# Kernel tuning notes

Measured on AMD Instinct MI355X. Metric: run time of the kernel, lower is better.

## Reference

```python
import jax, jax.numpy as jnp
import numpy as np
from jax import lax

V, E, H, T, B = 32000, 512, 512, 64, 64

def _xavier(key, shape):
    fan_out, fan_in = shape
    std = np.sqrt(2.0 / (fan_in + fan_out))
    return jax.random.normal(key, shape, dtype=jnp.float32) * std

def setup_inputs() -> dict:
    key = jax.random.key(0)
    ks = jax.random.split(key, 12)
    scale = np.sqrt(3.0 / E)
    emb = jax.random.uniform(ks[0], (V, E), minval=-scale, maxval=scale, dtype=jnp.float32)
    return {
        "emb": emb,                                   # frozen embedding table [V,E]
        "W_ih": _xavier(ks[1], (3 * H, E)),           # GRU input weights (r,z,n stacked)
        "W_hh": _xavier(ks[2], (3 * H, H)),           # GRU hidden weights
        "b_ih": jnp.zeros((3 * H,), jnp.float32),
        "b_hh": jnp.zeros((3 * H,), jnp.float32),
        "zt_W": _xavier(ks[3], (H, E + H)), "zt_b": jnp.zeros((H,), jnp.float32),
        "rt_W": _xavier(ks[4], (E, E + H)), "rt_b": jnp.zeros((E,), jnp.float32),
        "ht_W": _xavier(ks[5], (H, E + H)), "ht_b": jnp.zeros((H,), jnp.float32),
        "dec_W": _xavier(ks[6], (V, H)), "dec_b": jnp.zeros((V,), jnp.float32),
        "init_hidden": jnp.zeros((1, B, H), jnp.float32),
        "word": jax.random.randint(ks[7], (B,), 0, V),
        "seq": jax.random.randint(ks[8], (T, B), 0, V),
    }

def reference(emb, W_ih, W_hh, b_ih, b_hh, zt_W, zt_b, rt_W, rt_b, ht_W, ht_b,
              dec_W, dec_b, init_hidden, word, seq):
    word_emb = emb[word]          # [B,E] (frozen)
    seq_emb = emb[seq]            # [T,B,E]
    h0 = init_hidden[0]           # [B,H], single layer

    def step(h, x):
        # standard torch GRU cell
        gi = x @ W_ih.T + b_ih    # [B,3H]
        gh = h @ W_hh.T + b_hh
        i_r, i_z, i_n = jnp.split(gi, 3, axis=-1)
        h_r, h_z, h_n = jnp.split(gh, 3, axis=-1)
        r = jax.nn.sigmoid(i_r + h_r)
        z = jax.nn.sigmoid(i_z + h_z)
        n = jnp.tanh(i_n + r * h_n)
        h_gru = (1.0 - z) * n + z * h      # rnn output at this step
        # extra GRU-style gating with word embedding (use_g branch)
        inp_h = jnp.concatenate([word_emb, h_gru], axis=-1)      # [B,E+H]
        zt = jax.nn.sigmoid(inp_h @ zt_W.T + zt_b)               # [B,H]
        rt = jax.nn.sigmoid(inp_h @ rt_W.T + rt_b)               # [B,E]
        hcat = jnp.concatenate([rt * word_emb, h_gru], axis=-1)  # [B,E+H]
        h_tilde = jnp.tanh(hcat @ ht_W.T + ht_b)                 # [B,H]
        h_new = (1.0 - zt) * h_gru + zt * h_tilde
        return h_new, h_gru

    h_final, outs = lax.scan(step, h0, seq_emb)   # outs [T,B,H]
    flat = outs.reshape(-1, H)                    # [T*B,H]
    decoded = flat @ dec_W.T + dec_b              # [T*B,V]
    return decoded, h_final[None]                 # hidden [1,B,H]
```

## Files before the change

### kernel.cpp

```cpp
#include <hip/hip_runtime.h>
#include <stdint.h>

#define GAS __attribute__((address_space(1)))
#define LAS __attribute__((address_space(3)))

typedef __bf16 bf16x8 __attribute__((ext_vector_type(8)));
typedef _Float16 f16x8 __attribute__((ext_vector_type(8)));
typedef float f32x4 __attribute__((ext_vector_type(4)));

__device__ __forceinline__ unsigned short f2bf(float f) {
  unsigned u = __float_as_uint(f);
  unsigned r = (u + 0x7FFFu + ((u >> 16) & 1u)) >> 16;
  return (unsigned short)r;
}

__device__ __forceinline__ float sigmoidf(float x) {
  return 1.f / (1.f + expf(-x));
}

__device__ __forceinline__ void st2c(_Float16* p, _Float16 v) {
  unsigned short u = __builtin_bit_cast(unsigned short, v);
  __hip_atomic_store((unsigned short*)p, u, __ATOMIC_RELAXED, __HIP_MEMORY_SCOPE_AGENT);
}

__device__ __forceinline__ f16x8 ld8c(const _Float16* p) {
  unsigned long long a =
      __hip_atomic_load((const unsigned long long*)p, __ATOMIC_RELAXED, __HIP_MEMORY_SCOPE_AGENT);
  unsigned long long b =
      __hip_atomic_load((const unsigned long long*)(p + 4), __ATOMIC_RELAXED, __HIP_MEMORY_SCOPE_AGENT);
  union { unsigned long long u[2]; f16x8 v; } c;
  c.u[0] = a; c.u[1] = b;
  return c.v;
}

__global__ __launch_bounds__(128) void k_gather(
    const float* __restrict__ emb, const int* __restrict__ seq,
    const int* __restrict__ word, unsigned short* __restrict__ xbf,
    float* __restrict__ wemb) {
  int row = blockIdx.x;
  int tid = threadIdx.x;
  if (row < 4096) {
    const float* src = emb + (size_t)seq[row] * 512;
    unsigned short* dst = xbf + (size_t)row * 512;
    for (int e = tid; e < 512; e += 128) dst[e] = f2bf(src[e]);
  } else {
    int b = row - 4096;
    const float* src = emb + (size_t)word[b] * 512;
    float* dst = wemb + (size_t)b * 512;
    for (int e = tid; e < 512; e += 128) dst[e] = src[e];
  }
}

__global__ __launch_bounds__(128) void k_conv(
    const float* __restrict__ Wih, const float* __restrict__ decW,
    unsigned short* __restrict__ wih_bf, unsigned short* __restrict__ dec_bf) {
  int row = blockIdx.x;
  int tid = threadIdx.x;
  if (row < 1536) {
    const float* s = Wih + (size_t)row * 512;
    unsigned short* d = wih_bf + (size_t)row * 512;
    for (int e = tid; e < 512; e += 128) d[e] = f2bf(s[e]);
  } else {
    int o = row - 1536;
    const float* s = decW + (size_t)o * 512;
    unsigned short* d = dec_bf + (size_t)o * 512;
    for (int e = tid; e < 512; e += 128) d[e] = f2bf(s[e]);
  }
}

__global__ __launch_bounds__(256) void k_pre(
    const float* __restrict__ ztW, const float* __restrict__ ztb,
    const float* __restrict__ rtW, const float* __restrict__ rtb,
    const float* __restrict__ wemb, float* __restrict__ ztp,
    float* __restrict__ rtp) {
  int idx = blockIdx.x * 256 + threadIdx.x;
  int b = idx >> 10, o = idx & 1023;
  const float4* we = (const float4*)(wemb + (size_t)b * 512);
  const float4* wr;
  float acc;
  if (o < 512) { wr = (const float4*)(ztW + (size_t)o * 1024); acc = ztb[o]; }
  else { wr = (const float4*)(rtW + (size_t)(o - 512) * 1024); acc = rtb[o - 512]; }
  for (int c = 0; c < 128; ++c) {
    float4 w = wr[c], e = we[c];
    acc += w.x * e.x + w.y * e.y + w.z * e.z + w.w * e.w;
  }
  if (o < 512) ztp[(size_t)b * 512 + o] = acc;
  else rtp[(size_t)b * 512 + (o - 512)] = acc;
}

__global__ __launch_bounds__(256) void k_gemm_bt(
    const unsigned short* __restrict__ A, const unsigned short* __restrict__ B,
    float* __restrict__ C, const float* __restrict__ bias,
    int M, int N, int K) {
  __shared__ __align__(16) unsigned short As[128 * 32];
  __shared__ __align__(16) unsigned short Bs[128 * 32];
  int nt = N >> 7;
  int nwg = gridDim.x;
  int bid = blockIdx.x;
  int swz = (bid & 7) * (nwg >> 3) + (bid >> 3);
  int m0 = (swz / nt) << 7, n0 = (swz % nt) << 7;
  int tid = threadIdx.x;
  int l = tid & 63, w = tid >> 6;
  int wr = w >> 1, wc = w & 1;
  int lr = l & 15, lk = l >> 4;
  f32x4 acc[4][4] = {};
  for (int k0 = 0; k0 < K; k0 += 32) {
#pragma unroll
    for (int i = 0; i < 2; ++i) {
      int c = w * 2 + i;
      int off = c * 1024 + l * 16;
      int row = off >> 6, kb = off & 63;
      const char* ga = (const char*)A + ((size_t)(m0 + row) * K + k0) * 2 + kb;
      const char* gb = (const char*)B + ((size_t)(n0 + row) * K + k0) * 2 + kb;
      __builtin_amdgcn_global_load_lds((const GAS void*)ga,
                                       (LAS void*)((char*)As + c * 1024), 16, 0, 0);
      __builtin_amdgcn_global_load_lds((const GAS void*)gb,
                                       (LAS void*)((char*)Bs + c * 1024), 16, 0, 0);
    }
    asm volatile("s_waitcnt vmcnt(0)" ::: "memory");
    __syncthreads();
    bf16x8 af[4], bfr[4];
#pragma unroll
    for (int i = 0; i < 4; ++i)
      af[i] = *(const bf16x8*)&As[(wr * 64 + i * 16 + lr) * 32 + lk * 8];
#pragma unroll
    for (int i = 0; i < 4; ++i)
      bfr[i] = *(const bf16x8*)&Bs[(wc * 64 + i * 16 + lr) * 32 + lk * 8];
#pragma unroll
    for (int i = 0; i < 4; ++i)
#pragma unroll
      for (int jj = 0; jj < 4; ++jj)
        acc[i][jj] = __builtin_amdgcn_mfma_f32_16x16x32_bf16(af[i], bfr[jj], acc[i][jj], 0, 0, 0);
    __syncthreads();
  }
#pragma unroll
  for (int jj = 0; jj < 4; ++jj) {
    int col = n0 + wc * 64 + jj * 16 + lr;
    float bv = bias ? bias[col] : 0.f;
#pragma unroll
    for (int i = 0; i < 4; ++i) {
      int rb = m0 + wr * 64 + i * 16 + lk * 4;
#pragma unroll
      for (int q = 0; q < 4; ++q)
        C[(size_t)(rb + q) * N + col] = acc[i][jj][q] + bv;
    }
  }
}

struct RnnP {
  const float *Whh, *ztW, *rtW, *htW;
  const float *gi, *ztp, *rtp, *wemb, *inith, *bhh, *htb;
  _Float16 *hcur, *hgru, *rw;
  unsigned short *outsb;
  float *hfin;
  unsigned *bar;
};

__device__ __forceinline__ void gbar(unsigned* ctr, unsigned target) {
  asm volatile("s_waitcnt vmcnt(0)" ::: "memory");
  __syncthreads();
  if (threadIdx.x == 0) {
    __hip_atomic_fetch_add(ctr, 1u, __ATOMIC_RELAXED, __HIP_MEMORY_SCOPE_AGENT);
    while (__hip_atomic_load(ctr, __ATOMIC_RELAXED, __HIP_MEMORY_SCOPE_AGENT) < target)
      __builtin_amdgcn_s_sleep(4);
  }
  __syncthreads();
}

template <int NT>
__device__ __forceinline__ void mm_phase(f32x4* acc, const _Float16* A,
                                         const _Float16* WLrow, int w, int lr, int lk) {
  f16x8 af[16];
  const _Float16* arow = A + ((size_t)(16 * w + lr)) * 512 + lk * 8;
#pragma unroll
  for (int c = 0; c < 16; ++c) af[c] = ld8c(arow + c * 32);
#pragma unroll
  for (int c = 0; c < 16; ++c) {
#pragma unroll
    for (int n = 0; n < NT; ++n) {
      f16x8 bb = *(const f16x8*)(WLrow + (n * 16 + lr) * 520 + c * 32 + lk * 8);
      acc[n] = __builtin_amdgcn_mfma_f32_16x16x32_f16(af[c], bb, acc[n], 0, 0, 0);
    }
  }
}

__global__ __launch_bounds__(256) void k_rnn2(RnnP p) {
  const int g = blockIdx.x, tid = threadIdx.x;
  const int w = tid >> 6, l = tid & 63;
  const int lr = l & 15, lk = l >> 4;
  __shared__ _Float16 WL[112 * 520];
  for (int idx = tid; idx < 112 * 512; idx += 256) {
    int rr = idx >> 9, e = idx & 511;
    const float* src;
    if (rr < 48) {
      int gate = rr >> 4, i = rr & 15;
      src = p.Whh + ((size_t)(gate * 512 + g * 16 + i)) * 512 + e;
    } else if (rr < 96) {
      int r2 = rr - 48, gate = r2 >> 4, i = r2 & 15;
      const float* base = gate == 0 ? p.ztW : (gate == 1 ? p.rtW : p.htW);
      src = base + ((size_t)(g * 16 + i)) * 1024 + 512 + e;
    } else {
      int i = rr - 96;
      src = p.htW + ((size_t)(g * 16 + i)) * 1024 + e;
    }
    WL[rr * 520 + e] = (_Float16)(*src);
  }
  const int j = g * 16 + lr;
  const int brow = 16 * w + lk * 4;
  f32x4 hprev, zp, rp, wev;
#pragma unroll
  for (int q = 0; q < 4; ++q) {
    int b = brow + q;
    hprev[q] = p.inith[(size_t)b * 512 + j];
    zp[q] = p.ztp[(size_t)b * 512 + j];
    rp[q] = p.rtp[(size_t)b * 512 + j];
    wev[q] = p.wemb[(size_t)b * 512 + j];
    st2c(&p.hcur[(size_t)b * 512 + j], (_Float16)hprev[q]);
  }
  const float br = p.bhh[j], bz = p.bhh[512 + j], bn = p.bhh[1024 + j];
  const float bht = p.htb[j];
  float gir[12];
#pragma unroll
  for (int q = 0; q < 4; ++q) {
    const float* git = p.gi + (size_t)(brow + q) * 1536;
    gir[q * 3 + 0] = git[j];
    gir[q * 3 + 1] = git[512 + j];
    gir[q * 3 + 2] = git[1024 + j];
  }
  unsigned ord = 1;
  gbar(p.bar, 32 * ord); ord++;
  for (int t = 0; t < 64; ++t) {
    f32x4 acc1[3] = {};
    mm_phase<3>(acc1, p.hcur, &WL[0], w, lr, lk);
    f32x4 hg;
#pragma unroll
    for (int q = 0; q < 4; ++q) {
      int b = brow + q;
      float r = sigmoidf(gir[q * 3 + 0] + br + acc1[0][q]);
      float z = sigmoidf(gir[q * 3 + 1] + bz + acc1[1][q]);
      float n = tanhf(gir[q * 3 + 2] + r * (acc1[2][q] + bn));
      float hgq = (1.f - z) * n + z * hprev[q];
      hg[q] = hgq;
      st2c(&p.hgru[(size_t)b * 512 + j], (_Float16)hgq);
      p.outsb[((size_t)t * 64 + b) * 512 + j] = f2bf(hgq);
    }
    gbar(p.bar, 32 * ord); ord++;
    f32x4 acc2[3] = {};
    mm_phase<3>(acc2, p.hgru, &WL[48 * 520], w, lr, lk);
    f32x4 zt, htB;
#pragma unroll
    for (int q = 0; q < 4; ++q) {
      int b = brow + q;
      float ztq = sigmoidf(zp[q] + acc2[0][q]);
      float rtq = sigmoidf(rp[q] + acc2[1][q]);
      zt[q] = ztq;
      htB[q] = acc2[2][q];
      st2c(&p.rw[(size_t)b * 512 + j], (_Float16)(rtq * wev[q]));
    }
    gbar(p.bar, 32 * ord); ord++;
    if (t < 63) {
      const float* git = p.gi + (size_t)(t + 1) * 64 * 1536;
#pragma unroll
      for (int q = 0; q < 4; ++q) {
        const float* gb = git + (size_t)(brow + q) * 1536;
        gir[q * 3 + 0] = gb[j];
        gir[q * 3 + 1] = gb[512 + j];
        gir[q * 3 + 2] = gb[1024 + j];
      }
    }
    f32x4 acc3[1] = {};
    mm_phase<1>(acc3, p.rw, &WL[96 * 520], w, lr, lk);
#pragma unroll
    for (int q = 0; q < 4; ++q) {
      int b = brow + q;
      float htl = tanhf(acc3[0][q] + htB[q] + bht);
      float hn2 = (1.f - zt[q]) * hg[q] + zt[q] * htl;
      hprev[q] = hn2;
      if (t < 63) st2c(&p.hcur[(size_t)b * 512 + j], (_Float16)hn2);
      else p.hfin[(size_t)b * 512 + j] = hn2;
    }
    if (t < 63) { gbar(p.bar, 32 * ord); ord++; }
  }
}

extern "C" void kernel_launch(void* const* d_in, const int* in_sizes, int n_in,
                              void* d_out, int out_size, void* d_ws, size_t ws_size,
                              hipStream_t stream) {
  const float* emb   = (const float*)d_in[0];
  const float* Wih   = (const float*)d_in[1];
  const float* Whh   = (const float*)d_in[2];
  const float* bih   = (const float*)d_in[3];
  const float* bhh   = (const float*)d_in[4];
  const float* ztW   = (const float*)d_in[5];
  const float* ztb   = (const float*)d_in[6];
  const float* rtW   = (const float*)d_in[7];
  const float* rtb   = (const float*)d_in[8];
  const float* htW   = (const float*)d_in[9];
  const float* htb   = (const float*)d_in[10];
  const float* decW  = (const float*)d_in[11];
  const float* decb  = (const float*)d_in[12];
  const float* inith = (const float*)d_in[13];
  const int* word    = (const int*)d_in[14];
  const int* seq     = (const int*)d_in[15];
  float* out = (float*)d_out;

  char* ws = (char*)d_ws;
  size_t off = 0;
  auto alloc = [&](size_t bytes) {
    size_t o = off;
    off += (bytes + 255) & ~(size_t)255;
    return o;
  };
  unsigned short* xbf   = (unsigned short*)(ws + alloc(4096ull * 512 * 2));
  unsigned short* wihbf = (unsigned short*)(ws + alloc(1536ull * 512 * 2));
  unsigned short* decbf = (unsigned short*)(ws + alloc(32000ull * 512 * 2));
  float* wemb           = (float*)(ws + alloc(64ull * 512 * 4));
  float* ztp            = (float*)(ws + alloc(64ull * 512 * 4));
  float* rtp            = (float*)(ws + alloc(64ull * 512 * 4));
  float* gi             = (float*)(ws + alloc(4096ull * 1536 * 4));
  unsigned short* outsb = (unsigned short*)(ws + alloc(4096ull * 512 * 2));
  _Float16* hcur        = (_Float16*)(ws + alloc(64ull * 512 * 2));
  _Float16* hgru        = (_Float16*)(ws + alloc(64ull * 512 * 2));
  _Float16* rw          = (_Float16*)(ws + alloc(64ull * 512 * 2));
  unsigned* bar         = (unsigned*)(ws + alloc(256));

  hipLaunchKernelGGL(k_gather, dim3(4160), dim3(128), 0, stream,
                     emb, seq, word, xbf, wemb);
  hipLaunchKernelGGL(k_conv, dim3(33536), dim3(128), 0, stream,
                     Wih, decW, wihbf, decbf);
  hipLaunchKernelGGL(k_pre, dim3(256), dim3(256), 0, stream,
                     ztW, ztb, rtW, rtb, wemb, ztp, rtp);
  hipLaunchKernelGGL(k_gemm_bt, dim3(384), dim3(256), 0, stream,
                     xbf, wihbf, gi, bih, 4096, 1536, 512);
  hipMemsetAsync(bar, 0, 256, stream);
  RnnP p{Whh, ztW, rtW, htW, gi, ztp, rtp, wemb, inith, bhh, htb,
         hcur, hgru, rw, outsb, out + 4096ull * 32000, bar};
  hipLaunchKernelGGL(k_rnn2, dim3(32), dim3(256), 0, stream, p);
  hipLaunchKernelGGL(k_gemm_bt, dim3(8000), dim3(256), 0, stream,
                     outsb, decbf, out, decb, 4096, 32000, 512);
}
```

Baseline: 1.516 ms.

## Replace atomic-counter grid barrier with per-block flag array and wave-wide polling

The grid barrier in the persistent GRU kernel changes from a shared atomic counter that thread 0 polls with sleeps to per-block padded flags. Each block stores its phase, and every wave polls all 32 flags in parallel with a wave vote, so no atomic RMW contention and no extra __syncthreads remain. The hidden-state loads also become single 16-byte global_load_dwordx4 with sc0 sc1 cache bypass instead of two 8-byte atomic loads, with an explicit waitcnt before the MFMAs. This targets per-step sync latency in the 64-step recurrence. The memory-ordering guarantees rely on relaxed atomics and cache-bypass bits, which is a correctness risk.

```diff
diff --git a/kernel.cpp b/kernel.cpp
--- a/kernel.cpp
+++ b/kernel.cpp
@@ -23,14 +23,11 @@
   __hip_atomic_store((unsigned short*)p, u, __ATOMIC_RELAXED, __HIP_MEMORY_SCOPE_AGENT);
 }
 
-__device__ __forceinline__ f16x8 ld8c(const _Float16* p) {
-  unsigned long long a =
-      __hip_atomic_load((const unsigned long long*)p, __ATOMIC_RELAXED, __HIP_MEMORY_SCOPE_AGENT);
-  unsigned long long b =
-      __hip_atomic_load((const unsigned long long*)(p + 4), __ATOMIC_RELAXED, __HIP_MEMORY_SCOPE_AGENT);
-  union { unsigned long long u[2]; f16x8 v; } c;
-  c.u[0] = a; c.u[1] = b;
-  return c.v;
+__device__ __forceinline__ f16x8 ld16c(const _Float16* p) {
+  f32x4 r;
+  asm volatile("global_load_dwordx4 %0, %1, off sc0 sc1"
+               : "=v"(r) : "v"(p) : "memory");
+  return __builtin_bit_cast(f16x8, r);
 }
 
 __global__ __launch_bounds__(128) void k_gather(
@@ -153,18 +150,23 @@
   _Float16 *hcur, *hgru, *rw;
   unsigned short *outsb;
   float *hfin;
-  unsigned *bar;
+  unsigned *flags;
 };
 
-__device__ __forceinline__ void gbar(unsigned* ctr, unsigned target) {
+__device__ __forceinline__ void gbarf(unsigned* flags, int g, unsigned phase) {
   asm volatile("s_waitcnt vmcnt(0)" ::: "memory");
   __syncthreads();
-  if (threadIdx.x == 0) {
-    __hip_atomic_fetch_add(ctr, 1u, __ATOMIC_RELAXED, __HIP_MEMORY_SCOPE_AGENT);
-    while (__hip_atomic_load(ctr, __ATOMIC_RELAXED, __HIP_MEMORY_SCOPE_AGENT) < target)
-      __builtin_amdgcn_s_sleep(4);
-  }
-  __syncthreads();
+  if (threadIdx.x == 0)
+    __hip_atomic_store(flags + (size_t)g * 16, phase, __ATOMIC_RELAXED,
+                       __HIP_MEMORY_SCOPE_AGENT);
+  int lane = threadIdx.x & 63;
+  unsigned v;
+  do {
+    v = (lane < 32)
+            ? __hip_atomic_load(flags + (size_t)lane * 16, __ATOMIC_RELAXED,
+                                __HIP_MEMORY_SCOPE_AGENT)
+            : phase;
+  } while (!__all(v >= phase));
 }
 
 template <int NT>
@@ -173,7 +175,9 @@
   f16x8 af[16];
   const _Float16* arow = A + ((size_t)(16 * w + lr)) * 512 + lk * 8;
 #pragma unroll
-  for (int c = 0; c < 16; ++c) af[c] = ld8c(arow + c * 32);
+  for (int c = 0; c < 16; ++c) af[c] = ld16c(arow + c * 32);
+  asm volatile("s_waitcnt vmcnt(0)" ::: "memory");
+  __builtin_amdgcn_sched_barrier(0);
 #pragma unroll
   for (int c = 0; c < 16; ++c) {
 #pragma unroll
@@ -227,8 +231,8 @@
     gir[q * 3 + 1] = git[512 + j];
     gir[q * 3 + 2] = git[1024 + j];
   }
-  unsigned ord = 1;
-  gbar(p.bar, 32 * ord); ord++;
+  unsigned ph = 1;
+  gbarf(p.flags, g, ph); ph++;
   for (int t = 0; t < 64; ++t) {
     f32x4 acc1[3] = {};
     mm_phase<3>(acc1, p.hcur, &WL[0], w, lr, lk);
@@ -244,7 +248,7 @@
       st2c(&p.hgru[(size_t)b * 512 + j], (_Float16)hgq);
       p.outsb[((size_t)t * 64 + b) * 512 + j] = f2bf(hgq);
     }
-    gbar(p.bar, 32 * ord); ord++;
+    gbarf(p.flags, g, ph); ph++;
     f32x4 acc2[3] = {};
     mm_phase<3>(acc2, p.hgru, &WL[48 * 520], w, lr, lk);
     f32x4 zt, htB;
@@ -257,7 +261,7 @@
       htB[q] = acc2[2][q];
       st2c(&p.rw[(size_t)b * 512 + j], (_Float16)(rtq * wev[q]));
     }
-    gbar(p.bar, 32 * ord); ord++;
+    gbarf(p.flags, g, ph); ph++;
     if (t < 63) {
       const float* git = p.gi + (size_t)(t + 1) * 64 * 1536;
 #pragma unroll
@@ -279,7 +283,7 @@
       if (t < 63) st2c(&p.hcur[(size_t)b * 512 + j], (_Float16)hn2);
       else p.hfin[(size_t)b * 512 + j] = hn2;
     }
-    if (t < 63) { gbar(p.bar, 32 * ord); ord++; }
+    if (t < 63) { gbarf(p.flags, g, ph); ph++; }
   }
 }
 
@@ -322,7 +326,7 @@
   _Float16* hcur        = (_Float16*)(ws + alloc(64ull * 512 * 2));
   _Float16* hgru        = (_Float16*)(ws + alloc(64ull * 512 * 2));
   _Float16* rw          = (_Float16*)(ws + alloc(64ull * 512 * 2));
-  unsigned* bar         = (unsigned*)(ws + alloc(256));
+  unsigned* flags       = (unsigned*)(ws + alloc(32 * 64));
 
   hipLaunchKernelGGL(k_gather, dim3(4160), dim3(128), 0, stream,
                      emb, seq, word, xbf, wemb);
@@ -332,9 +336,9 @@
                      ztW, ztb, rtW, rtb, wemb, ztp, rtp);
   hipLaunchKernelGGL(k_gemm_bt, dim3(384), dim3(256), 0, stream,
                      xbf, wihbf, gi, bih, 4096, 1536, 512);
-  hipMemsetAsync(bar, 0, 256, stream);
+  hipMemsetAsync(flags, 0, 32 * 64, stream);
   RnnP p{Whh, ztW, rtW, htW, gi, ztp, rtp, wemb, inith, bhh, htb,
-         hcur, hgru, rw, outsb, out + 4096ull * 32000, bar};
+         hcur, hgru, rw, outsb, out + 4096ull * 32000, flags};
   hipLaunchKernelGGL(k_rnn2, dim3(32), dim3(256), 0, stream, p);
   hipLaunchKernelGGL(k_gemm_bt, dim3(8000), dim3(256), 0, stream,
                      outsb, decbf, out, decb, 4096, 32000, 512);
```

Result: faster. 1.326 ms (-12.5%).

## Replace grid barriers with tagged dataflow polling in persistent GRU kernel

Applied to the files above, without the earlier changes.

Drops the atomic-counter global barrier between recurrent phases. Each fp16 value is now stored in a 32-bit word whose upper half carries a step/phase tag, and consumers spin-load their operand rows with cache-bypassing dwordx4 loads until every tag matches. This removes the full-grid synchronization latency per phase, at the cost of doubling the operand traffic and relying on tag monotonicity. The tagged buffers must be zeroed by a memset before launch.

```diff
diff --git a/kernel.cpp b/kernel.cpp
--- a/kernel.cpp
+++ b/kernel.cpp
@@ -7,6 +7,7 @@
 typedef __bf16 bf16x8 __attribute__((ext_vector_type(8)));
 typedef _Float16 f16x8 __attribute__((ext_vector_type(8)));
 typedef float f32x4 __attribute__((ext_vector_type(4)));
+typedef unsigned u32x4 __attribute__((ext_vector_type(4)));
 
 __device__ __forceinline__ unsigned short f2bf(float f) {
   unsigned u = __float_as_uint(f);
@@ -18,19 +19,21 @@
   return 1.f / (1.f + expf(-x));
 }
 
-__device__ __forceinline__ void st2c(_Float16* p, _Float16 v) {
-  unsigned short u = __builtin_bit_cast(unsigned short, v);
-  __hip_atomic_store((unsigned short*)p, u, __ATOMIC_RELAXED, __HIP_MEMORY_SCOPE_AGENT);
-}
-
-__device__ __forceinline__ f16x8 ld8c(const _Float16* p) {
-  unsigned long long a =
-      __hip_atomic_load((const unsigned long long*)p, __ATOMIC_RELAXED, __HIP_MEMORY_SCOPE_AGENT);
-  unsigned long long b =
-      __hip_atomic_load((const unsigned long long*)(p + 4), __ATOMIC_RELAXED, __HIP_MEMORY_SCOPE_AGENT);
-  union { unsigned long long u[2]; f16x8 v; } c;
-  c.u[0] = a; c.u[1] = b;
-  return c.v;
+__device__ __forceinline__ unsigned f16bits(float x) {
+  _Float16 h = (_Float16)x;
+  return (unsigned)__builtin_bit_cast(unsigned short, h);
+}
+
+__device__ __forceinline__ void st1c(unsigned* p, unsigned v) {
+  __hip_atomic_store(p, v, __ATOMIC_RELAXED, __HIP_MEMORY_SCOPE_AGENT);
+}
+
+template <int OFF>
+__device__ __forceinline__ u32x4 ld4c(const unsigned* p) {
+  u32x4 r;
+  asm volatile("global_load_dwordx4 %0, %1, off offset:%2 sc0 sc1"
+               : "=v"(r) : "v"(p), "n"(OFF) : "memory");
+  return r;
 }
 
 __global__ __launch_bounds__(128) void k_gather(
@@ -150,41 +153,53 @@
 struct RnnP {
   const float *Whh, *ztW, *rtW, *htW;
   const float *gi, *ztp, *rtp, *wemb, *inith, *bhh, *htb;
-  _Float16 *hcur, *hgru, *rw;
+  unsigned *hcurT, *hgruT, *rwT;
   unsigned short *outsb;
   float *hfin;
-  unsigned *bar;
 };
 
-__device__ __forceinline__ void gbar(unsigned* ctr, unsigned target) {
-  asm volatile("s_waitcnt vmcnt(0)" ::: "memory");
-  __syncthreads();
-  if (threadIdx.x == 0) {
-    __hip_atomic_fetch_add(ctr, 1u, __ATOMIC_RELAXED, __HIP_MEMORY_SCOPE_AGENT);
-    while (__hip_atomic_load(ctr, __ATOMIC_RELAXED, __HIP_MEMORY_SCOPE_AGENT) < target)
-      __builtin_amdgcn_s_sleep(4);
-  }
-  __syncthreads();
-}
-
 template <int NT>
-__device__ __forceinline__ void mm_phase(f32x4* acc, const _Float16* A,
-                                         const _Float16* WLrow, int w, int lr, int lk) {
-  f16x8 af[16];
-  const _Float16* arow = A + ((size_t)(16 * w + lr)) * 512 + lk * 8;
-#pragma unroll
-  for (int c = 0; c < 16; ++c) af[c] = ld8c(arow + c * 32);
+__device__ __forceinline__ void mm_poll(f32x4* acc, const unsigned* At,
+                                        const _Float16* WLrow, unsigned tag,
+                                        int w, int lr, int lk) {
+  u32x4 raw[32];
+  const unsigned* arow = At + ((size_t)(16 * w + lr)) * 512 + lk * 8;
+  const unsigned texp = tag << 16;
+  for (;;) {
+#define LD2(c) \
+    raw[2 * (c)] = ld4c<(c) * 128>(arow); \
+    raw[2 * (c) + 1] = ld4c<(c) * 128 + 16>(arow);
+    LD2(0) LD2(1) LD2(2) LD2(3) LD2(4) LD2(5) LD2(6) LD2(7)
+    LD2(8) LD2(9) LD2(10) LD2(11) LD2(12) LD2(13) LD2(14) LD2(15)
+#undef LD2
+    asm volatile("s_waitcnt vmcnt(0)" ::: "memory");
+    __builtin_amdgcn_sched_barrier(0);
+    unsigned bad = 0;
+#pragma unroll
+    for (int i = 0; i < 32; ++i) {
+      u32x4 v = raw[i];
+      bad |= (v.x ^ texp) | (v.y ^ texp) | (v.z ^ texp) | (v.w ^ texp);
+    }
+    if (__all((int)((bad >> 16) == 0u))) break;
+  }
+  __builtin_amdgcn_sched_barrier(0);
 #pragma unroll
   for (int c = 0; c < 16; ++c) {
+    unsigned p0 = __builtin_amdgcn_perm(raw[2 * c].y, raw[2 * c].x, 0x05040100);
+    unsigned p1 = __builtin_amdgcn_perm(raw[2 * c].w, raw[2 * c].z, 0x05040100);
+    unsigned p2 = __builtin_amdgcn_perm(raw[2 * c + 1].y, raw[2 * c + 1].x, 0x05040100);
+    unsigned p3 = __builtin_amdgcn_perm(raw[2 * c + 1].w, raw[2 * c + 1].z, 0x05040100);
+    u32x4 pk = {p0, p1, p2, p3};
+    f16x8 a = __builtin_bit_cast(f16x8, pk);
 #pragma unroll
     for (int n = 0; n < NT; ++n) {
       f16x8 bb = *(const f16x8*)(WLrow + (n * 16 + lr) * 520 + c * 32 + lk * 8);
-      acc[n] = __builtin_amdgcn_mfma_f32_16x16x32_f16(af[c], bb, acc[n], 0, 0, 0);
-    }
-  }
-}
-
-__global__ __launch_bounds__(256) void k_rnn2(RnnP p) {
+      acc[n] = __builtin_amdgcn_mfma_f32_16x16x32_f16(a, bb, acc[n], 0, 0, 0);
+    }
+  }
+}
+
+__global__ __launch_bounds__(256, 1) void k_rnn3(RnnP p) {
   const int g = blockIdx.x, tid = threadIdx.x;
   const int w = tid >> 6, l = tid & 63;
   const int lr = l & 15, lk = l >> 4;
@@ -205,6 +220,7 @@
     }
     WL[rr * 520 + e] = (_Float16)(*src);
   }
+  __syncthreads();
   const int j = g * 16 + lr;
   const int brow = 16 * w + lk * 4;
   f32x4 hprev, zp, rp, wev;
@@ -215,7 +231,6 @@
     zp[q] = p.ztp[(size_t)b * 512 + j];
     rp[q] = p.rtp[(size_t)b * 512 + j];
     wev[q] = p.wemb[(size_t)b * 512 + j];
-    st2c(&p.hcur[(size_t)b * 512 + j], (_Float16)hprev[q]);
   }
   const float br = p.bhh[j], bz = p.bhh[512 + j], bn = p.bhh[1024 + j];
   const float bht = p.htb[j];
@@ -227,11 +242,13 @@
     gir[q * 3 + 1] = git[512 + j];
     gir[q * 3 + 2] = git[1024 + j];
   }
-  unsigned ord = 1;
-  gbar(p.bar, 32 * ord); ord++;
+#pragma unroll
+  for (int q = 0; q < 4; ++q)
+    st1c(&p.hcurT[(size_t)(brow + q) * 512 + j], (3u << 16) | f16bits(hprev[q]));
   for (int t = 0; t < 64; ++t) {
+    const unsigned tg = 3u * (unsigned)t;
     f32x4 acc1[3] = {};
-    mm_phase<3>(acc1, p.hcur, &WL[0], w, lr, lk);
+    mm_poll<3>(acc1, p.hcurT, &WL[0], tg + 3, w, lr, lk);
     f32x4 hg;
 #pragma unroll
     for (int q = 0; q < 4; ++q) {
@@ -241,12 +258,11 @@
       float n = tanhf(gir[q * 3 + 2] + r * (acc1[2][q] + bn));
       float hgq = (1.f - z) * n + z * hprev[q];
       hg[q] = hgq;
-      st2c(&p.hgru[(size_t)b * 512 + j], (_Float16)hgq);
+      st1c(&p.hgruT[(size_t)b * 512 + j], ((tg + 4) << 16) | f16bits(hgq));
       p.outsb[((size_t)t * 64 + b) * 512 + j] = f2bf(hgq);
     }
-    gbar(p.bar, 32 * ord); ord++;
     f32x4 acc2[3] = {};
-    mm_phase<3>(acc2, p.hgru, &WL[48 * 520], w, lr, lk);
+    mm_poll<3>(acc2, p.hgruT, &WL[48 * 520], tg + 4, w, lr, lk);
     f32x4 zt, htB;
 #pragma unroll
     for (int q = 0; q < 4; ++q) {
@@ -255,9 +271,8 @@
       float rtq = sigmoidf(rp[q] + acc2[1][q]);
       zt[q] = ztq;
       htB[q] = acc2[2][q];
-      st2c(&p.rw[(size_t)b * 512 + j], (_Float16)(rtq * wev[q]));
-    }
-    gbar(p.bar, 32 * ord); ord++;
+      st1c(&p.rwT[(size_t)b * 512 + j], ((tg + 5) << 16) | f16bits(rtq * wev[q]));
+    }
     if (t < 63) {
       const float* git = p.gi + (size_t)(t + 1) * 64 * 1536;
 #pragma unroll
@@ -269,17 +284,16 @@
       }
     }
     f32x4 acc3[1] = {};
-    mm_phase<1>(acc3, p.rw, &WL[96 * 520], w, lr, lk);
+    mm_poll<1>(acc3, p.rwT, &WL[96 * 520], tg + 5, w, lr, lk);
 #pragma unroll
     for (int q = 0; q < 4; ++q) {
       int b = brow + q;
       float htl = tanhf(acc3[0][q] + htB[q] + bht);
       float hn2 = (1.f - zt[q]) * hg[q] + zt[q] * htl;
       hprev[q] = hn2;
-      if (t < 63) st2c(&p.hcur[(size_t)b * 512 + j], (_Float16)hn2);
+      if (t < 63) st1c(&p.hcurT[(size_t)b * 512 + j], ((tg + 6) << 16) | f16bits(hn2));
       else p.hfin[(size_t)b * 512 + j] = hn2;
     }
-    if (t < 63) { gbar(p.bar, 32 * ord); ord++; }
   }
 }
 
@@ -319,10 +333,9 @@
   float* rtp            = (float*)(ws + alloc(64ull * 512 * 4));
   float* gi             = (float*)(ws + alloc(4096ull * 1536 * 4));
   unsigned short* outsb = (unsigned short*)(ws + alloc(4096ull * 512 * 2));
-  _Float16* hcur        = (_Float16*)(ws + alloc(64ull * 512 * 2));
-  _Float16* hgru        = (_Float16*)(ws + alloc(64ull * 512 * 2));
-  _Float16* rw          = (_Float16*)(ws + alloc(64ull * 512 * 2));
-  unsigned* bar         = (unsigned*)(ws + alloc(256));
+  unsigned* hcurT       = (unsigned*)(ws + alloc(64ull * 512 * 4));
+  unsigned* hgruT       = (unsigned*)(ws + alloc(64ull * 512 * 4));
+  unsigned* rwT         = (unsigned*)(ws + alloc(64ull * 512 * 4));
 
   hipLaunchKernelGGL(k_gather, dim3(4160), dim3(128), 0, stream,
                      emb, seq, word, xbf, wemb);
@@ -332,10 +345,10 @@
                      ztW, ztb, rtW, rtb, wemb, ztp, rtp);
   hipLaunchKernelGGL(k_gemm_bt, dim3(384), dim3(256), 0, stream,
                      xbf, wihbf, gi, bih, 4096, 1536, 512);
-  hipMemsetAsync(bar, 0, 256, stream);
+  hipMemsetAsync(hcurT, 0, 3ull * 64 * 512 * 4, stream);
   RnnP p{Whh, ztW, rtW, htW, gi, ztp, rtp, wemb, inith, bhh, htb,
-         hcur, hgru, rw, outsb, out + 4096ull * 32000, bar};
-  hipLaunchKernelGGL(k_rnn2, dim3(32), dim3(256), 0, stream, p);
+         hcurT, hgruT, rwT, outsb, out + 4096ull * 32000};
+  hipLaunchKernelGGL(k_rnn3, dim3(32), dim3(256), 0, stream, p);
   hipLaunchKernelGGL(k_gemm_bt, dim3(8000), dim3(256), 0, stream,
                      outsb, decbf, out, decb, 4096, 32000, 512);
 }
```

New measurement: 1.929 ms. 1.27x slower.
